# Kernel tuning notes

Measured on AMD Instinct MI355X. Metric: run time of the kernel, lower is better.

Reference implementation:

```python
import jax, jax.numpy as jnp
import numpy as np

B, T, S, C, H = 4, 1024, 1024, 1024, 16
D = C // H  # head_dim = 64


def rms_norm(x, scale):
    # matches torch RMSNorm: float32 compute, eps=1e-6, learned scale
    rr = jax.lax.rsqrt(jnp.mean(x * x, axis=-1, keepdims=True) + 1e-6)
    return x * rr * scale


def setup_inputs() -> dict:
    key = jax.random.key(0)
    ks = jax.random.split(key, 12)
    s = 0.02
    return {
        "x": jax.random.normal(ks[0], (B, T, C), jnp.float32),
        "encoder_output": jax.random.normal(ks[1], (B, S, C), jnp.float32),
        "Wq": jax.random.normal(ks[2], (C, C), jnp.float32) * s,
        "bq": jnp.zeros((C,), jnp.float32),
        "Wk": jax.random.normal(ks[3], (C, C), jnp.float32) * s,
        "bk": jnp.zeros((C,), jnp.float32),
        "Wv": jax.random.normal(ks[4], (C, C), jnp.float32) * s,
        "bv": jnp.zeros((C,), jnp.float32),
        "q_scale": jnp.ones((C,), jnp.float32),
        "k_scale": jnp.ones((C,), jnp.float32),
        "Wp": jax.random.normal(ks[5], (C, C), jnp.float32) * s,
        "bp": jnp.zeros((C,), jnp.float32),
    }


def reference(x, encoder_output, Wq, bq, Wk, bk, Wv, bv, q_scale, k_scale, Wp, bp):
    # projections (dropout layers are identity in eval)
    q = x @ Wq + bq                      # [B,T,C]
    k = encoder_output @ Wk + bk         # [B,S,C]
    v = encoder_output @ Wv + bv         # [B,S,C]
    # RMSNorm + residual on q and k
    q = rms_norm(q, q_scale) + q
    k = rms_norm(k, k_scale) + k
    # split heads -> [B,H,T,D] / [B,H,S,D]
    qh = q.reshape(B, T, H, D).transpose(0, 2, 1, 3)
    kh = k.reshape(B, S, H, D).transpose(0, 2, 1, 3)
    vh = v.reshape(B, S, H, D).transpose(0, 2, 1, 3)
    scale = D ** -0.5
    scores = jnp.einsum('bhtd,bhsd->bhts', qh, kh) * scale  # [B,H,T,S]
    attn = jax.nn.softmax(scores, axis=-1)
    y = jnp.einsum('bhts,bhsd->bhtd', attn, vh)             # [B,H,T,D]
    y = y.transpose(0, 2, 1, 3).reshape(B, T, C)
    y = y @ Wp + bp
    attn_mean = attn.mean(axis=1)                            # [B,T,S]
    return (y, attn_mean)
```

## Files before the change

### kernel.cpp

```cpp
#include <hip/hip_runtime.h>
#include <hip/hip_bf16.h>
#include <stdint.h>

typedef __attribute__((ext_vector_type(8))) __bf16 bf16x8;
typedef __attribute__((ext_vector_type(4))) float f32x4;

#define MFMA16(a,b,c) __builtin_amdgcn_mfma_f32_16x16x32_bf16((a),(b),(c),0,0,0)

__device__ __forceinline__ unsigned short f2bf(float f) {
  unsigned int u = __float_as_uint(f);
  u += 0x7fffu + ((u >> 16) & 1u);
  return (unsigned short)(u >> 16);
}
__device__ __forceinline__ float bf2f(unsigned short s) {
  return __uint_as_float(((unsigned int)s) << 16);
}

__device__ __forceinline__ void gl_lds16(const void* g, void* l) {
  __builtin_amdgcn_global_load_lds((const __attribute__((address_space(1))) void*)g,
                                   (__attribute__((address_space(3))) void*)l, 16, 0, 0);
}

__global__ __launch_bounds__(256) void cvt_bf16_kernel(const float* __restrict__ in,
                                                       unsigned short* __restrict__ out, int n4) {
  int i = blockIdx.x * 256 + threadIdx.x;
  if (i < n4) {
    float4 v = ((const float4*)in)[i];
    ushort4 o; o.x = f2bf(v.x); o.y = f2bf(v.y); o.z = f2bf(v.z); o.w = f2bf(v.w);
    ((ushort4*)out)[i] = o;
  }
}

__global__ __launch_bounds__(256) void transpose_cvt_kernel(const float* __restrict__ src,
                                                            unsigned short* __restrict__ dst) {
  __shared__ float tile[64][65];
  const int N = 1024;
  size_t zoff = (size_t)blockIdx.z * N * N;
  int r0 = blockIdx.y * 64, c0 = blockIdx.x * 64;
  int t = threadIdx.x;
  int cc = t & 63, rr = t >> 6;
#pragma unroll
  for (int i = 0; i < 16; i++)
    tile[rr + i*4][cc] = src[zoff + (size_t)(r0 + rr + i*4) * N + c0 + cc];
  __syncthreads();
#pragma unroll
  for (int i = 0; i < 16; i++)
    dst[zoff + (size_t)(c0 + rr + i*4) * N + r0 + cc] = f2bf(tile[cc][rr + i*4]);
}

__global__ __launch_bounds__(256) void rmsnorm_res_kernel(const float* __restrict__ raw,
                                                          const float* __restrict__ scale,
                                                          unsigned short* __restrict__ out) {
  int row = blockIdx.x, t = threadIdx.x;
  float4 v = ((const float4*)(raw + (size_t)row * 1024))[t];
  float ss = v.x*v.x + v.y*v.y + v.z*v.z + v.w*v.w;
#pragma unroll
  for (int off = 32; off > 0; off >>= 1) ss += __shfl_down(ss, off);
  __shared__ float red[4];
  if ((t & 63) == 0) red[t >> 6] = ss;
  __syncthreads();
  float rr = rsqrtf((red[0] + red[1] + red[2] + red[3]) * (1.0f/1024.0f) + 1e-6f);
  float4 sc = ((const float4*)scale)[t];
  ushort4 o;
  o.x = f2bf(v.x * (rr*sc.x + 1.0f));
  o.y = f2bf(v.y * (rr*sc.y + 1.0f));
  o.z = f2bf(v.z * (rr*sc.z + 1.0f));
  o.w = f2bf(v.w * (rr*sc.w + 1.0f));
  ((ushort4*)(out + (size_t)row * 1024))[t] = o;
}

__global__ __launch_bounds__(256) void gemm_bt_kernel(const unsigned short* __restrict__ A,
                                                      const unsigned short* __restrict__ Bt,
                                                      const float* __restrict__ bias,
                                                      float* __restrict__ C,
                                                      int M, int N, int K) {
  __shared__ __align__(16) unsigned short sA[128 * 32];
  __shared__ __align__(16) unsigned short sB[64 * 32];
  const int tid = threadIdx.x;
  const int wave = tid >> 6, lane = tid & 63;
  const int m0 = blockIdx.y * 128, n0 = blockIdx.x * 64;
  const int wm = (wave >> 1) * 64, wn = (wave & 1) * 32;
  const int lr = lane & 15, lg = lane >> 4;
  const int srow = lane >> 2;
  const int scol = (lane & 3) * 16;

  f32x4 acc[4][2];
#pragma unroll
  for (int i = 0; i < 4; i++)
#pragma unroll
    for (int j = 0; j < 2; j++) acc[i][j] = (f32x4){0.f, 0.f, 0.f, 0.f};

  for (int k0 = 0; k0 < K; k0 += 32) {
    __syncthreads();
#pragma unroll
    for (int j = 0; j < 2; j++) {
      int row = j * 64 + wave * 16 + srow;
      gl_lds16((const char*)(A + (size_t)(m0 + row) * K + k0) + scol,
               (char*)sA + (j * 64 + wave * 16) * 64);
    }
    {
      int row = wave * 16 + srow;
      gl_lds16((const char*)(Bt + (size_t)(n0 + row) * K + k0) + scol,
               (char*)sB + (wave * 16) * 64);
    }
    __syncthreads();
    bf16x8 a[4], bb[2];
#pragma unroll
    for (int mf = 0; mf < 4; mf++)
      a[mf] = *(const bf16x8*)((const char*)sA + ((wm + mf * 16 + lr) * 32 + lg * 8) * 2);
#pragma unroll
    for (int nf = 0; nf < 2; nf++)
      bb[nf] = *(const bf16x8*)((const char*)sB + ((wn + nf * 16 + lr) * 32 + lg * 8) * 2);
#pragma unroll
    for (int mf = 0; mf < 4; mf++)
#pragma unroll
      for (int nf = 0; nf < 2; nf++)
        acc[mf][nf] = MFMA16(a[mf], bb[nf], acc[mf][nf]);
  }
#pragma unroll
  for (int nf = 0; nf < 2; nf++) {
    int col = n0 + wn + nf * 16 + lr;
    float bv = bias[col];
#pragma unroll
    for (int mf = 0; mf < 4; mf++)
#pragma unroll
      for (int r = 0; r < 4; r++) {
        int row = m0 + wm + mf * 16 + lg * 4 + r;
        C[(size_t)row * N + col] = acc[mf][nf][r] + bv;
      }
  }
}

__global__ __launch_bounds__(1024) void attn_kernel(const unsigned short* __restrict__ qbf,
                                                    const unsigned short* __restrict__ kbf,
                                                    const unsigned short* __restrict__ vt,
                                                    unsigned short* __restrict__ ybf,
                                                    float* __restrict__ am) {
  const int b = blockIdx.x >> 6;
  const int t0 = (blockIdx.x & 63) * 16;
  const int h = threadIdx.x >> 6;
  const int lane = threadIdx.x & 63;
  const int lr = lane & 15, lg = lane >> 4;

  __shared__ unsigned short P_lds[16][16][72];
  __shared__ float invl_lds[16][16];

  const unsigned short* qb = qbf + ((size_t)(b * 1024 + t0 + lr)) * 1024 + h * 64 + lg * 8;
  bf16x8 qf0 = *(const bf16x8*)qb;
  bf16x8 qf1 = *(const bf16x8*)(qb + 32);

  const size_t kbase = (size_t)b * 1024 * 1024;
  float m[4] = {-1e30f, -1e30f, -1e30f, -1e30f};
  float lsum[4] = {0.f, 0.f, 0.f, 0.f};

  for (int s0 = 0; s0 < 1024; s0 += 32) {
    const unsigned short* kp = kbf + kbase + (size_t)(s0 + lr) * 1024 + h * 64 + lg * 8;
    bf16x8 k00 = *(const bf16x8*)kp;
    bf16x8 k01 = *(const bf16x8*)(kp + 32);
    bf16x8 k10 = *(const bf16x8*)(kp + 16 * 1024);
    bf16x8 k11 = *(const bf16x8*)(kp + 16 * 1024 + 32);
    f32x4 sa = {0.f,0.f,0.f,0.f}, sb = {0.f,0.f,0.f,0.f};
    sa = MFMA16(qf0, k00, sa); sa = MFMA16(qf1, k01, sa);
    sb = MFMA16(qf0, k10, sb); sb = MFMA16(qf1, k11, sb);
#pragma unroll
    for (int r = 0; r < 4; r++) {
      float v0 = sa[r] * 0.125f, v1 = sb[r] * 0.125f;
      float tm = fmaxf(v0, v1);
      tm = fmaxf(tm, __shfl_xor(tm, 1));
      tm = fmaxf(tm, __shfl_xor(tm, 2));
      tm = fmaxf(tm, __shfl_xor(tm, 4));
      tm = fmaxf(tm, __shfl_xor(tm, 8));
      float mn = fmaxf(m[r], tm);
      float ps = __expf(v0 - mn) + __expf(v1 - mn);
      ps += __shfl_xor(ps, 1); ps += __shfl_xor(ps, 2);
      ps += __shfl_xor(ps, 4); ps += __shfl_xor(ps, 8);
      lsum[r] = lsum[r] * __expf(m[r] - mn) + ps;
      m[r] = mn;
    }
  }
  float invl[4];
#pragma unroll
  for (int r = 0; r < 4; r++) invl[r] = 1.0f / lsum[r];
  if (lr == 0) {
#pragma unroll
    for (int r = 0; r < 4; r++) invl_lds[h][lg * 4 + r] = invl[r];
  }
  f32x4 yacc[4];
#pragma unroll
  for (int i = 0; i < 4; i++) yacc[i] = (f32x4){0.f, 0.f, 0.f, 0.f};
  __syncthreads();

  for (int s0 = 0; s0 < 1024; s0 += 32) {
    const unsigned short* kp = kbf + kbase + (size_t)(s0 + lr) * 1024 + h * 64 + lg * 8;
    bf16x8 k00 = *(const bf16x8*)kp;
    bf16x8 k01 = *(const bf16x8*)(kp + 32);
    bf16x8 k10 = *(const bf16x8*)(kp + 16 * 1024);
    bf16x8 k11 = *(const bf16x8*)(kp + 16 * 1024 + 32);
    f32x4 sa = {0.f,0.f,0.f,0.f}, sb = {0.f,0.f,0.f,0.f};
    sa = MFMA16(qf0, k00, sa); sa = MFMA16(qf1, k01, sa);
    sb = MFMA16(qf0, k10, sb); sb = MFMA16(qf1, k11, sb);
#pragma unroll
    for (int r = 0; r < 4; r++) {
      float p0 = __expf(sa[r] * 0.125f - m[r]);
      float p1 = __expf(sb[r] * 0.125f - m[r]);
      P_lds[h][lg * 4 + r][lr] = f2bf(p0);
      P_lds[h][lg * 4 + r][16 + lr] = f2bf(p1);
    }
    __syncthreads();
    {
      int e = (int)threadIdx.x;
      if (e < 512) {
        int tt = e >> 5, ssx = e & 31;
        float a = 0.f;
#pragma unroll
        for (int hh = 0; hh < 16; hh++)
          a += bf2f(P_lds[hh][tt][ssx]) * invl_lds[hh][tt];
        am[((size_t)(b * 1024 + t0 + tt)) * 1024 + s0 + ssx] = a * 0.0625f;
      }
    }
    bf16x8 pf = *(const bf16x8*)&P_lds[h][lr][lg * 8];
    const unsigned short* vb = vt + ((size_t)(b * 1024 + h * 64 + lr)) * 1024 + s0 + lg * 8;
#pragma unroll
    for (int nf = 0; nf < 4; nf++) {
      bf16x8 vf = *(const bf16x8*)(vb + (size_t)nf * 16 * 1024);
      yacc[nf] = MFMA16(pf, vf, yacc[nf]);
    }
    __syncthreads();
  }
#pragma unroll
  for (int nf = 0; nf < 4; nf++)
#pragma unroll
    for (int r = 0; r < 4; r++) {
      float yv = yacc[nf][r] * invl[r];
      ybf[((size_t)(b * 1024 + t0 + lg * 4 + r)) * 1024 + h * 64 + nf * 16 + lr] = f2bf(yv);
    }
}

extern "C" void kernel_launch(void* const* d_in, const int* in_sizes, int n_in,
                              void* d_out, int out_size, void* d_ws, size_t ws_size,
                              hipStream_t stream) {
  const float* x   = (const float*)d_in[0];
  const float* enc = (const float*)d_in[1];
  const float* Wq  = (const float*)d_in[2];
  const float* bq  = (const float*)d_in[3];
  const float* Wk  = (const float*)d_in[4];
  const float* bk  = (const float*)d_in[5];
  const float* Wv  = (const float*)d_in[6];
  const float* bv  = (const float*)d_in[7];
  const float* qs  = (const float*)d_in[8];
  const float* ks  = (const float*)d_in[9];
  const float* Wp  = (const float*)d_in[10];
  const float* bp  = (const float*)d_in[11];

  float* y_out = (float*)d_out;
  float* am    = (float*)d_out + (size_t)4*1024*1024;

  char* ws = (char*)d_ws;
  unsigned short* xb  = (unsigned short*)(ws);
  unsigned short* eb  = (unsigned short*)(ws + ((size_t)8  << 20));
  unsigned short* Wqt = (unsigned short*)(ws + ((size_t)16 << 20));
  unsigned short* Wkt = (unsigned short*)(ws + ((size_t)18 << 20));
  unsigned short* Wvt = (unsigned short*)(ws + ((size_t)20 << 20));
  unsigned short* Wpt = (unsigned short*)(ws + ((size_t)22 << 20));
  unsigned short* qb  = (unsigned short*)(ws + ((size_t)24 << 20));
  unsigned short* kb  = (unsigned short*)(ws + ((size_t)32 << 20));
  unsigned short* vt  = (unsigned short*)(ws + ((size_t)40 << 20));
  unsigned short* yb  = (unsigned short*)(ws + ((size_t)48 << 20));
  float* raw          = (float*)(ws + ((size_t)56 << 20));

  const int M = 4096, N = 1024, K = 1024;

  cvt_bf16_kernel<<<4096, 256, 0, stream>>>(x,   xb, 1024 * 1024);
  cvt_bf16_kernel<<<4096, 256, 0, stream>>>(enc, eb, 1024 * 1024);

  dim3 tg(16, 16, 1);
  transpose_cvt_kernel<<<tg, 256, 0, stream>>>(Wq, Wqt);
  transpose_cvt_kernel<<<tg, 256, 0, stream>>>(Wk, Wkt);
  transpose_cvt_kernel<<<tg, 256, 0, stream>>>(Wv, Wvt);
  transpose_cvt_kernel<<<tg, 256, 0, stream>>>(Wp, Wpt);

  dim3 gg(N / 64, M / 128);
  gemm_bt_kernel<<<gg, 256, 0, stream>>>(xb, Wqt, bq, raw, M, N, K);
  rmsnorm_res_kernel<<<4096, 256, 0, stream>>>(raw, qs, qb);
  gemm_bt_kernel<<<gg, 256, 0, stream>>>(eb, Wkt, bk, raw, M, N, K);
  rmsnorm_res_kernel<<<4096, 256, 0, stream>>>(raw, ks, kb);
  gemm_bt_kernel<<<gg, 256, 0, stream>>>(eb, Wvt, bv, raw, M, N, K);
  dim3 tg4(16, 16, 4);
  transpose_cvt_kernel<<<tg4, 256, 0, stream>>>(raw, vt);

  attn_kernel<<<256, 1024, 0, stream>>>(qb, kb, vt, yb, am);

  gemm_bt_kernel<<<gg, 256, 0, stream>>>(yb, Wpt, bp, y_out, M, N, K);
}
```

Baseline: 414.9 us.

## Split attention into single-pass per-head blocks plus separate head-mean kernel

The attention kernel becomes one 64-thread block per (batch, head, 16-row tile) and makes a single pass over keys instead of two. It drops the running-max subtraction, which assumes the scaled scores never overflow exp. Each block writes its unnormalized bf16 probabilities and inverse row sums to a large global buffer. A new kernel then reads them back to form the head-averaged attention map. This removes the block-wide __syncthreads and the duplicate QK pass, at the cost of a large extra global write and read of P and a numerical-range risk. The workspace layout is reorganized, with a per-batch fallback when the workspace is small.

```diff
diff --git a/kernel.cpp b/kernel.cpp
--- a/kernel.cpp
+++ b/kernel.cpp
@@ -131,30 +131,38 @@
   }
 }
 
-__global__ __launch_bounds__(1024) void attn_kernel(const unsigned short* __restrict__ qbf,
-                                                    const unsigned short* __restrict__ kbf,
-                                                    const unsigned short* __restrict__ vt,
-                                                    unsigned short* __restrict__ ybf,
-                                                    float* __restrict__ am) {
-  const int b = blockIdx.x >> 6;
-  const int t0 = (blockIdx.x & 63) * 16;
-  const int h = threadIdx.x >> 6;
-  const int lane = threadIdx.x & 63;
+__global__ __launch_bounds__(64) void attn_kernel(const unsigned short* __restrict__ qbf,
+                                                  const unsigned short* __restrict__ kbf,
+                                                  const unsigned short* __restrict__ vt,
+                                                  unsigned short* __restrict__ ybf,
+                                                  unsigned short* __restrict__ Pg,
+                                                  float* __restrict__ invl_g,
+                                                  int b_base) {
+  const int h    = blockIdx.x & 15;
+  const int tt   = (blockIdx.x >> 4) & 63;
+  const int bloc = blockIdx.x >> 10;
+  const int b    = b_base + bloc;
+  const int t0   = tt * 16;
+  const int lane = threadIdx.x;
   const int lr = lane & 15, lg = lane >> 4;
 
-  __shared__ unsigned short P_lds[16][16][72];
-  __shared__ float invl_lds[16][16];
-
-  const unsigned short* qb = qbf + ((size_t)(b * 1024 + t0 + lr)) * 1024 + h * 64 + lg * 8;
-  bf16x8 qf0 = *(const bf16x8*)qb;
-  bf16x8 qf1 = *(const bf16x8*)(qb + 32);
-
-  const size_t kbase = (size_t)b * 1024 * 1024;
-  float m[4] = {-1e30f, -1e30f, -1e30f, -1e30f};
+  __shared__ __align__(16) unsigned short P_lds[16][40];
+
+  const unsigned short* qp = qbf + ((size_t)(b * 1024 + t0 + lr)) * 1024 + h * 64 + lg * 8;
+  bf16x8 qf0 = *(const bf16x8*)qp;
+  bf16x8 qf1 = *(const bf16x8*)(qp + 32);
+
+  const unsigned short* kbase = kbf + (size_t)b * 1024 * 1024 + (size_t)lr * 1024 + h * 64 + lg * 8;
+  const unsigned short* vrow0 = vt + ((size_t)(b * 1024 + h * 64 + lr)) * 1024 + lg * 8;
+  unsigned short* pout = Pg + (((size_t)(bloc * 16 + h) * 1024) + t0 + (lane >> 2)) * 1024 + (lane & 3) * 8;
+
   float lsum[4] = {0.f, 0.f, 0.f, 0.f};
+  f32x4 yacc[4];
+#pragma unroll
+  for (int i = 0; i < 4; i++) yacc[i] = (f32x4){0.f, 0.f, 0.f, 0.f};
 
   for (int s0 = 0; s0 < 1024; s0 += 32) {
-    const unsigned short* kp = kbf + kbase + (size_t)(s0 + lr) * 1024 + h * 64 + lg * 8;
+    const unsigned short* kp = kbase + (size_t)s0 * 1024;
     bf16x8 k00 = *(const bf16x8*)kp;
     bf16x8 k01 = *(const bf16x8*)(kp + 32);
     bf16x8 k10 = *(const bf16x8*)(kp + 16 * 1024);
@@ -164,76 +172,65 @@
     sb = MFMA16(qf0, k10, sb); sb = MFMA16(qf1, k11, sb);
 #pragma unroll
     for (int r = 0; r < 4; r++) {
-      float v0 = sa[r] * 0.125f, v1 = sb[r] * 0.125f;
-      float tm = fmaxf(v0, v1);
-      tm = fmaxf(tm, __shfl_xor(tm, 1));
-      tm = fmaxf(tm, __shfl_xor(tm, 2));
-      tm = fmaxf(tm, __shfl_xor(tm, 4));
-      tm = fmaxf(tm, __shfl_xor(tm, 8));
-      float mn = fmaxf(m[r], tm);
-      float ps = __expf(v0 - mn) + __expf(v1 - mn);
-      ps += __shfl_xor(ps, 1); ps += __shfl_xor(ps, 2);
-      ps += __shfl_xor(ps, 4); ps += __shfl_xor(ps, 8);
-      lsum[r] = lsum[r] * __expf(m[r] - mn) + ps;
-      m[r] = mn;
-    }
+      float p0 = __expf(sa[r] * 0.125f);
+      float p1 = __expf(sb[r] * 0.125f);
+      lsum[r] += p0 + p1;
+      P_lds[lg * 4 + r][lr]      = f2bf(p0);
+      P_lds[lg * 4 + r][16 + lr] = f2bf(p1);
+    }
+    bf16x8 pf = *(const bf16x8*)&P_lds[lr][lg * 8];
+#pragma unroll
+    for (int nf = 0; nf < 4; nf++) {
+      bf16x8 vf = *(const bf16x8*)(vrow0 + (size_t)nf * 16 * 1024 + s0);
+      yacc[nf] = MFMA16(pf, vf, yacc[nf]);
+    }
+    bf16x8 prow = *(const bf16x8*)&P_lds[lane >> 2][(lane & 3) * 8];
+    *(bf16x8*)(pout + s0) = prow;
+  }
+#pragma unroll
+  for (int r = 0; r < 4; r++) {
+    float v = lsum[r];
+    v += __shfl_xor(v, 1); v += __shfl_xor(v, 2);
+    v += __shfl_xor(v, 4); v += __shfl_xor(v, 8);
+    lsum[r] = v;
   }
   float invl[4];
 #pragma unroll
   for (int r = 0; r < 4; r++) invl[r] = 1.0f / lsum[r];
   if (lr == 0) {
 #pragma unroll
-    for (int r = 0; r < 4; r++) invl_lds[h][lg * 4 + r] = invl[r];
-  }
-  f32x4 yacc[4];
-#pragma unroll
-  for (int i = 0; i < 4; i++) yacc[i] = (f32x4){0.f, 0.f, 0.f, 0.f};
+    for (int r = 0; r < 4; r++)
+      invl_g[((size_t)(b * 16 + h)) * 1024 + t0 + lg * 4 + r] = invl[r];
+  }
+#pragma unroll
+  for (int nf = 0; nf < 4; nf++)
+#pragma unroll
+    for (int r = 0; r < 4; r++)
+      ybf[((size_t)(b * 1024 + t0 + lg * 4 + r)) * 1024 + h * 64 + nf * 16 + lr] =
+          f2bf(yacc[nf][r] * invl[r]);
+}
+
+__global__ __launch_bounds__(256) void am_kernel(const unsigned short* __restrict__ Pg,
+                                                 const float* __restrict__ invl_g,
+                                                 float* __restrict__ am, int b_base) {
+  const int trow = blockIdx.x & 1023;
+  const int bloc = blockIdx.x >> 10;
+  const int b    = b_base + bloc;
+  __shared__ float il[16];
+  if (threadIdx.x < 16)
+    il[threadIdx.x] = invl_g[((size_t)(b * 16 + threadIdx.x)) * 1024 + trow];
   __syncthreads();
-
-  for (int s0 = 0; s0 < 1024; s0 += 32) {
-    const unsigned short* kp = kbf + kbase + (size_t)(s0 + lr) * 1024 + h * 64 + lg * 8;
-    bf16x8 k00 = *(const bf16x8*)kp;
-    bf16x8 k01 = *(const bf16x8*)(kp + 32);
-    bf16x8 k10 = *(const bf16x8*)(kp + 16 * 1024);
-    bf16x8 k11 = *(const bf16x8*)(kp + 16 * 1024 + 32);
-    f32x4 sa = {0.f,0.f,0.f,0.f}, sb = {0.f,0.f,0.f,0.f};
-    sa = MFMA16(qf0, k00, sa); sa = MFMA16(qf1, k01, sa);
-    sb = MFMA16(qf0, k10, sb); sb = MFMA16(qf1, k11, sb);
-#pragma unroll
-    for (int r = 0; r < 4; r++) {
-      float p0 = __expf(sa[r] * 0.125f - m[r]);
-      float p1 = __expf(sb[r] * 0.125f - m[r]);
-      P_lds[h][lg * 4 + r][lr] = f2bf(p0);
-      P_lds[h][lg * 4 + r][16 + lr] = f2bf(p1);
-    }
-    __syncthreads();
-    {
-      int e = (int)threadIdx.x;
-      if (e < 512) {
-        int tt = e >> 5, ssx = e & 31;
-        float a = 0.f;
-#pragma unroll
-        for (int hh = 0; hh < 16; hh++)
-          a += bf2f(P_lds[hh][tt][ssx]) * invl_lds[hh][tt];
-        am[((size_t)(b * 1024 + t0 + tt)) * 1024 + s0 + ssx] = a * 0.0625f;
-      }
-    }
-    bf16x8 pf = *(const bf16x8*)&P_lds[h][lr][lg * 8];
-    const unsigned short* vb = vt + ((size_t)(b * 1024 + h * 64 + lr)) * 1024 + s0 + lg * 8;
-#pragma unroll
-    for (int nf = 0; nf < 4; nf++) {
-      bf16x8 vf = *(const bf16x8*)(vb + (size_t)nf * 16 * 1024);
-      yacc[nf] = MFMA16(pf, vf, yacc[nf]);
-    }
-    __syncthreads();
-  }
-#pragma unroll
-  for (int nf = 0; nf < 4; nf++)
-#pragma unroll
-    for (int r = 0; r < 4; r++) {
-      float yv = yacc[nf][r] * invl[r];
-      ybf[((size_t)(b * 1024 + t0 + lg * 4 + r)) * 1024 + h * 64 + nf * 16 + lr] = f2bf(yv);
-    }
+  const int sc = threadIdx.x * 4;
+  float a0 = 0.f, a1 = 0.f, a2 = 0.f, a3 = 0.f;
+#pragma unroll
+  for (int hh = 0; hh < 16; hh++) {
+    ushort4 pv = *(const ushort4*)(Pg + (((size_t)(bloc * 16 + hh) * 1024) + trow) * 1024 + sc);
+    float w = il[hh];
+    a0 += bf2f(pv.x) * w; a1 += bf2f(pv.y) * w;
+    a2 += bf2f(pv.z) * w; a3 += bf2f(pv.w) * w;
+  }
+  float4 o = {a0 * 0.0625f, a1 * 0.0625f, a2 * 0.0625f, a3 * 0.0625f};
+  *(float4*)(am + ((size_t)(b * 1024) + trow) * 1024 + sc) = o;
 }
 
 extern "C" void kernel_launch(void* const* d_in, const int* in_sizes, int n_in,
@@ -256,17 +253,41 @@
   float* am    = (float*)d_out + (size_t)4*1024*1024;
 
   char* ws = (char*)d_ws;
-  unsigned short* xb  = (unsigned short*)(ws);
-  unsigned short* eb  = (unsigned short*)(ws + ((size_t)8  << 20));
-  unsigned short* Wqt = (unsigned short*)(ws + ((size_t)16 << 20));
-  unsigned short* Wkt = (unsigned short*)(ws + ((size_t)18 << 20));
-  unsigned short* Wvt = (unsigned short*)(ws + ((size_t)20 << 20));
-  unsigned short* Wpt = (unsigned short*)(ws + ((size_t)22 << 20));
-  unsigned short* qb  = (unsigned short*)(ws + ((size_t)24 << 20));
-  unsigned short* kb  = (unsigned short*)(ws + ((size_t)32 << 20));
-  unsigned short* vt  = (unsigned short*)(ws + ((size_t)40 << 20));
-  unsigned short* yb  = (unsigned short*)(ws + ((size_t)48 << 20));
-  float* raw          = (float*)(ws + ((size_t)56 << 20));
+  const size_t MB = (size_t)1 << 20;
+  const size_t NEED_BIG = 163 * MB;
+  const bool big = (ws_size >= NEED_BIG);
+
+  unsigned short *P, *xb, *eb, *Wqt, *Wkt, *Wvt, *Wpt, *qb, *kb, *vtp, *yb;
+  float *raw, *invl;
+  if (big) {
+    P    = (unsigned short*)(ws);
+    xb   = (unsigned short*)(ws);
+    eb   = (unsigned short*)(ws + 8*MB);
+    raw  = (float*)        (ws + 16*MB);
+    Wqt  = (unsigned short*)(ws + 32*MB);
+    Wkt  = (unsigned short*)(ws + 34*MB);
+    Wvt  = (unsigned short*)(ws + 36*MB);
+    Wpt  = (unsigned short*)(ws + 128*MB);
+    qb   = (unsigned short*)(ws + 130*MB);
+    kb   = (unsigned short*)(ws + 138*MB);
+    vtp  = (unsigned short*)(ws + 146*MB);
+    yb   = (unsigned short*)(ws + 154*MB);
+    invl = (float*)        (ws + 162*MB);
+  } else {
+    P    = (unsigned short*)(ws);
+    xb   = (unsigned short*)(ws);
+    eb   = (unsigned short*)(ws + 8*MB);
+    raw  = (float*)        (ws + 16*MB);
+    Wqt  = (unsigned short*)(ws + 32*MB);
+    Wkt  = (unsigned short*)(ws + 34*MB);
+    Wvt  = (unsigned short*)(ws + 36*MB);
+    Wpt  = (unsigned short*)(ws + 38*MB);
+    qb   = (unsigned short*)(ws + 40*MB);
+    kb   = (unsigned short*)(ws + 48*MB);
+    vtp  = (unsigned short*)(ws + 56*MB);
+    yb   = (unsigned short*)(ws + 64*MB);
+    invl = (float*)        (ws + 72*MB);
+  }
 
   const int M = 4096, N = 1024, K = 1024;
 
@@ -286,9 +307,17 @@
   rmsnorm_res_kernel<<<4096, 256, 0, stream>>>(raw, ks, kb);
   gemm_bt_kernel<<<gg, 256, 0, stream>>>(eb, Wvt, bv, raw, M, N, K);
   dim3 tg4(16, 16, 4);
-  transpose_cvt_kernel<<<tg4, 256, 0, stream>>>(raw, vt);
-
-  attn_kernel<<<256, 1024, 0, stream>>>(qb, kb, vt, yb, am);
+  transpose_cvt_kernel<<<tg4, 256, 0, stream>>>(raw, vtp);
+
+  if (big) {
+    attn_kernel<<<4096, 64, 0, stream>>>(qb, kb, vtp, yb, P, invl, 0);
+    am_kernel<<<4096, 256, 0, stream>>>(P, invl, am, 0);
+  } else {
+    for (int b = 0; b < 4; b++) {
+      attn_kernel<<<1024, 64, 0, stream>>>(qb, kb, vtp, yb, P, invl, b);
+      am_kernel<<<1024, 256, 0, stream>>>(P, invl, am, b);
+    }
+  }
 
   gemm_bt_kernel<<<gg, 256, 0, stream>>>(yb, Wpt, bp, y_out, M, N, K);
 }
```

After: 382.6 us. -7.8%, faster.
